# Performance work log

Hardware: AMD Instinct MI355X
Metric: run time of the kernel (lower is better)

Reference implementation:

```python
import jax, jax.numpy as jnp
import numpy as np

B = 256      # batch
D_IN = 784   # input_dims
WIDTH = 256  # block width
DEPTH = 10   # number of fc_relu blocks
NCLS = 10    # num_classes


def setup_inputs() -> dict:
    key = jax.random.key(0)
    ks = jax.random.split(key, 7)
    s1 = 1.0 / np.sqrt(D_IN)
    s2 = 1.0 / np.sqrt(WIDTH)
    x = jax.random.normal(ks[0], (B, D_IN), jnp.float32)
    W1 = jax.random.uniform(ks[1], (WIDTH, D_IN), jnp.float32, -s1, s1)
    b1 = jax.random.uniform(ks[2], (WIDTH,), jnp.float32, -s1, s1)
    Wb = jax.random.uniform(ks[3], (DEPTH, WIDTH, WIDTH), jnp.float32, -s2, s2)
    bb = jax.random.uniform(ks[4], (DEPTH, WIDTH), jnp.float32, -s2, s2)
    Wl = jax.random.uniform(ks[5], (NCLS, WIDTH), jnp.float32, -s2, s2)
    bl = jax.random.uniform(ks[6], (NCLS,), jnp.float32, -s2, s2)
    return dict(x=x, W1=W1, b1=b1, Wb=Wb, bb=bb, Wl=Wl, bl=bl)


def reference(x, W1, b1, Wb, bb, Wl, bl):
    # first_fc + relu
    y = jax.nn.relu(x @ W1.T + b1)                      # [B, WIDTH]
    eye = jnp.eye(WIDTH, dtype=y.dtype)

    def step(y, wb):
        W, b = wb                                       # [WIDTH, WIDTH], [WIDTH]
        # fc_relu.dev(x, skip=True): per-sample Jacobian W @ diag(relu'(x)) + I
        # (W @ diag(d) scales columns of W by d) -- vectorized replacement for
        # the original nested Python-loop diag build.
        mask = (y >= 0).astype(y.dtype)                 # [B, WIDTH]
        J = W[None, :, :] * mask[:, None, :] + eye      # [B, WIDTH, WIDTH]
        sigma = jnp.linalg.svd(J, compute_uv=False)     # [B, WIDTH], descending
        # residual relu block: relu(fc(x)) + x
        y = jax.nn.relu(y @ W.T + b) + y
        return y, sigma

    y, sigmas = jax.lax.scan(step, y, (Wb, bb))         # sigmas: [DEPTH, B, WIDTH]
    # feat_tag='ldi': all_sigma = mean over blocks of sigma_mean
    all_sigma = jnp.mean(sigmas, axis=0)                # [B, WIDTH]
    out = y @ Wl.T + bl                                 # last_fc, [B, NCLS]
    return out, all_sigma
```

## Files before the change

### kernel.cpp

```cpp
#include <hip/hip_runtime.h>
#include <hip/hip_bf16.h>

#define NW 256
#define NDEPTH 10
#define NS 25
#define PAD 12
#define PIV_EPS 1e-6f

__global__ __launch_bounds__(256) void bmat_fwd_kernel(
    const float* __restrict__ Wb, float* __restrict__ Ball, unsigned int* __restrict__ rsmax,
    const float* __restrict__ x, const float* __restrict__ W1, const float* __restrict__ b1,
    const float* __restrict__ bb, const float* __restrict__ Wl, const float* __restrict__ bl,
    float* __restrict__ out) {
  __shared__ __align__(16) float xs[784];
  __shared__ __align__(16) float ybuf[2][NW];
  __shared__ float wsum[4][8];

  if (blockIdx.x < NDEPTH * 32) {
    const int blk = blockIdx.x;
    const int k   = blk >> 5;
    const int r0  = (blk & 31) << 3;
    const int c   = threadIdx.x;
    const float* W = Wb + (size_t)k * NW * NW;
    float acc[8] = {0.f,0.f,0.f,0.f,0.f,0.f,0.f,0.f};
    for (int j = 0; j < NW; ++j) {
      const float wc = W[j * NW + c];
#pragma unroll
      for (int rr = 0; rr < 8; ++rr) acc[rr] += wc * W[j * NW + r0 + rr];
    }
    float a[8];
#pragma unroll
    for (int rr = 0; rr < 8; ++rr) {
      const int r = r0 + rr;
      const float s = acc[rr] + W[c * NW + r] + W[r * NW + c] + ((r == c) ? 1.f : 0.f);
      Ball[(size_t)k * NW * NW + r * NW + c] = s;
      a[rr] = fabsf(s);
    }
#pragma unroll
    for (int off = 32; off; off >>= 1) {
#pragma unroll
      for (int rr = 0; rr < 8; ++rr) a[rr] += __shfl_down(a[rr], off);
    }
    if ((c & 63) == 0) {
#pragma unroll
      for (int rr = 0; rr < 8; ++rr) wsum[c >> 6][rr] = a[rr];
    }
    __syncthreads();
    if (c == 0) {
      float mx = 0.f;
#pragma unroll
      for (int rr = 0; rr < 8; ++rr)
        mx = fmaxf(mx, wsum[0][rr] + wsum[1][rr] + wsum[2][rr] + wsum[3][rr]);
      atomicMax(&rsmax[k], __float_as_uint(mx));
    }
  } else {
    const int b = blockIdx.x - NDEPTH * 32;
    const int o = threadIdx.x;
    for (int k = o; k < 784; k += 256) xs[k] = x[(size_t)b * 784 + k];
    __syncthreads();
    {
      const float* w1r = W1 + (size_t)o * 784;
      float a0 = 0.f, a1 = 0.f, a2 = 0.f, a3 = 0.f;
      for (int k = 0; k < 784; k += 16) {
        const float4 w0 = *(const float4*)(w1r + k);
        const float4 x0 = *(const float4*)(&xs[k]);
        const float4 w1v = *(const float4*)(w1r + k + 4);
        const float4 x1 = *(const float4*)(&xs[k + 4]);
        const float4 w2 = *(const float4*)(w1r + k + 8);
        const float4 x2 = *(const float4*)(&xs[k + 8]);
        const float4 w3 = *(const float4*)(w1r + k + 12);
        const float4 x3 = *(const float4*)(&xs[k + 12]);
        a0 += w0.x*x0.x + w0.y*x0.y + w0.z*x0.z + w0.w*x0.w;
        a1 += w1v.x*x1.x + w1v.y*x1.y + w1v.z*x1.z + w1v.w*x1.w;
        a2 += w2.x*x2.x + w2.y*x2.y + w2.z*x2.z + w2.w*x2.w;
        a3 += w3.x*x3.x + w3.y*x3.y + w3.z*x3.z + w3.w*x3.w;
      }
      ybuf[0][o] = fmaxf(b1[o] + ((a0 + a1) + (a2 + a3)), 0.f);
    }
    __syncthreads();
    int cur = 0;
    for (int d = 0; d < NDEPTH; ++d) {
      const float* wr = Wb + (size_t)d * NW * NW + (size_t)o * NW;
      const float* yc = ybuf[cur];
      float a0 = 0.f, a1 = 0.f, a2 = 0.f, a3 = 0.f;
#pragma unroll 4
      for (int k = 0; k < NW; k += 16) {
        const float4 w0 = *(const float4*)(wr + k);
        const float4 y0 = *(const float4*)(&yc[k]);
        const float4 w1v = *(const float4*)(wr + k + 4);
        const float4 y1 = *(const float4*)(&yc[k + 4]);
        const float4 w2 = *(const float4*)(wr + k + 8);
        const float4 y2 = *(const float4*)(&yc[k + 8]);
        const float4 w3 = *(const float4*)(wr + k + 12);
        const float4 y3 = *(const float4*)(&yc[k + 12]);
        a0 += w0.x*y0.x + w0.y*y0.y + w0.z*y0.z + w0.w*y0.w;
        a1 += w1v.x*y1.x + w1v.y*y1.y + w1v.z*y1.z + w1v.w*y1.w;
        a2 += w2.x*y2.x + w2.y*y2.y + w2.z*y2.z + w2.w*y2.w;
        a3 += w3.x*y3.x + w3.y*y3.y + w3.z*y3.z + w3.w*y3.w;
      }
      const float acc = bb[d * NW + o] + ((a0 + a1) + (a2 + a3));
      const float ynew = fmaxf(acc, 0.f) + yc[o];
      ybuf[cur ^ 1][o] = ynew;
      __syncthreads();
      cur ^= 1;
    }
    if (o < 10) {
      const float* wr = Wl + o * NW;
      const float* yc = ybuf[cur];
      float a0 = 0.f, a1 = 0.f;
      for (int k = 0; k < NW; k += 8) {
        const float4 w0 = *(const float4*)(wr + k);
        const float4 y0 = *(const float4*)(&yc[k]);
        const float4 w1v = *(const float4*)(wr + k + 4);
        const float4 y1 = *(const float4*)(&yc[k + 4]);
        a0 += w0.x*y0.x + w0.y*y0.y + w0.z*y0.z + w0.w*y0.w;
        a1 += w1v.x*y1.x + w1v.y*y1.y + w1v.z*y1.z + w1v.w*y1.w;
      }
      out[b * 10 + o] = bl[o] + a0 + a1;
    }
  }
}

__global__ __launch_bounds__(1024, 4) void ldl_kernel(const float* __restrict__ Ball,
                                                      const unsigned int* __restrict__ rsmax,
                                                      int* __restrict__ counts) {
  const int s   = blockIdx.x;
  const int mat = blockIdx.y;
  const int t = threadIdx.x;
  const int l = t & 63;
  const int w = t >> 6;
  const int rg = l & 31;
  const int ch = 2 * w + (l >> 5);
  const int r0 = rg << 3;

  __shared__ __align__(16) float vrow[2][2][32 * PAD];

  const float h = sqrtf(__uint_as_float(rsmax[mat])) * (1.f / NS);
  const float sg = (s + 1) * h;
  const float mu = sg * sg;

  float Bf[64];
  {
    const float* src = Ball + (size_t)mat * NW * NW + (size_t)r0 * NW + (ch << 3);
#pragma unroll
    for (int i = 0; i < 8; ++i) {
      const float4 a = *(const float4*)(src + i * NW);
      const float4 b = *(const float4*)(src + i * NW + 4);
      Bf[i*8+0] = a.x; Bf[i*8+1] = a.y; Bf[i*8+2] = a.z; Bf[i*8+3] = a.w;
      Bf[i*8+4] = b.x; Bf[i*8+5] = b.y; Bf[i*8+6] = b.z; Bf[i*8+7] = b.w;
    }
  }
  if (rg == ch) {
#pragma unroll
    for (int i = 0; i < 8; ++i) Bf[i*8+i] -= mu;
  }

  if (rg == 0) {
    float* vd0 = &vrow[0][0][ch * PAD];
    float* vd1 = &vrow[0][1][ch * PAD];
    *(float4*)&vd0[0] = make_float4(Bf[0],  Bf[1],  Bf[2],  Bf[3]);
    *(float4*)&vd0[4] = make_float4(Bf[4],  Bf[5],  Bf[6],  Bf[7]);
    *(float4*)&vd1[0] = make_float4(Bf[8],  Bf[9],  Bf[10], Bf[11]);
    *(float4*)&vd1[4] = make_float4(Bf[12], Bf[13], Bf[14], Bf[15]);
  }
  __syncthreads();

  int cnt = 0;
  for (int m = 0; m < NW / 2; ++m) {
    const int k = 2 * m;
    const int par = m & 1;
    const float* v0 = vrow[par][0];
    const float* v1 = vrow[par][1];

    const int kpos = (k >> 3) * PAD + (k & 7);
    const float2 p01 = *(const float2*)&v0[kpos];
    const float d0  = p01.x;
    const float u01 = p01.y;
    const float e1  = v1[kpos + 1];
    const float d0g = (fabsf(d0) < PIV_EPS) ? copysignf(PIV_EPS, d0) : d0;
    const float i0  = __builtin_amdgcn_rcpf(d0g);
    const float l10 = u01 * i0;
    const float d1  = e1 - l10 * u01;
    const float d1g = (fabsf(d1) < PIV_EPS) ? copysignf(PIV_EPS, d1) : d1;
    const float i1  = __builtin_amdgcn_rcpf(d1g);
    cnt += (d0 < 0.f) ? 1 : 0;
    cnt += (d1 < 0.f) ? 1 : 0;

    if (16 * w + 15 > k) {
      const float4 ra0 = *(const float4*)&v0[rg * PAD + 0];
      const float4 ra1 = *(const float4*)&v0[rg * PAD + 4];
      const float4 rb0 = *(const float4*)&v1[rg * PAD + 0];
      const float4 rb1 = *(const float4*)&v1[rg * PAD + 4];
      const float4 ca0 = *(const float4*)&v0[ch * PAD + 0];
      const float4 ca1 = *(const float4*)&v0[ch * PAD + 4];
      const float4 cb0 = *(const float4*)&v1[ch * PAD + 0];
      const float4 cb1 = *(const float4*)&v1[ch * PAD + 4];
      const float rv0[8] = {ra0.x, ra0.y, ra0.z, ra0.w, ra1.x, ra1.y, ra1.z, ra1.w};
      const float rv1[8] = {rb0.x, rb0.y, rb0.z, rb0.w, rb1.x, rb1.y, rb1.z, rb1.w};
      const float cv0[8] = {ca0.x, ca0.y, ca0.z, ca0.w, ca1.x, ca1.y, ca1.z, ca1.w};
      const float cv1[8] = {cb0.x, cb0.y, cb0.z, cb0.w, cb1.x, cb1.y, cb1.z, cb1.w};

      float g0[8], f1[8];
#pragma unroll
      for (int i = 0; i < 8; ++i) {
        const int r = r0 + i;
        const float f0 = (r > k)     ? -rv0[i] * i0 : 0.f;
        const float v1p = rv1[i] - l10 * rv0[i];
        f1[i] = (r > k + 1) ? -v1p * i1 : 0.f;
        g0[i] = f0 - l10 * f1[i];
      }
#pragma unroll
      for (int i = 0; i < 8; ++i) {
#pragma unroll
        for (int j = 0; j < 8; ++j) {
          Bf[i*8+j] = fmaf(g0[i], cv0[j], fmaf(f1[i], cv1[j], Bf[i*8+j]));
        }
      }
      const int nr = k + 2;
      if (nr < NW && rg == (nr >> 3)) {
        float* vd0 = &vrow[par ^ 1][0][ch * PAD];
        float* vd1 = &vrow[par ^ 1][1][ch * PAD];
        switch (nr & 7) {
          case 0:
            *(float4*)&vd0[0] = make_float4(Bf[0],  Bf[1],  Bf[2],  Bf[3]);
            *(float4*)&vd0[4] = make_float4(Bf[4],  Bf[5],  Bf[6],  Bf[7]);
            *(float4*)&vd1[0] = make_float4(Bf[8],  Bf[9],  Bf[10], Bf[11]);
            *(float4*)&vd1[4] = make_float4(Bf[12], Bf[13], Bf[14], Bf[15]);
            break;
          case 2:
            *(float4*)&vd0[0] = make_float4(Bf[16], Bf[17], Bf[18], Bf[19]);
            *(float4*)&vd0[4] = make_float4(Bf[20], Bf[21], Bf[22], Bf[23]);
            *(float4*)&vd1[0] = make_float4(Bf[24], Bf[25], Bf[26], Bf[27]);
            *(float4*)&vd1[4] = make_float4(Bf[28], Bf[29], Bf[30], Bf[31]);
            break;
          case 4:
            *(float4*)&vd0[0] = make_float4(Bf[32], Bf[33], Bf[34], Bf[35]);
            *(float4*)&vd0[4] = make_float4(Bf[36], Bf[37], Bf[38], Bf[39]);
            *(float4*)&vd1[0] = make_float4(Bf[40], Bf[41], Bf[42], Bf[43]);
            *(float4*)&vd1[4] = make_float4(Bf[44], Bf[45], Bf[46], Bf[47]);
            break;
          default:
            *(float4*)&vd0[0] = make_float4(Bf[48], Bf[49], Bf[50], Bf[51]);
            *(float4*)&vd0[4] = make_float4(Bf[52], Bf[53], Bf[54], Bf[55]);
            *(float4*)&vd1[0] = make_float4(Bf[56], Bf[57], Bf[58], Bf[59]);
            *(float4*)&vd1[4] = make_float4(Bf[60], Bf[61], Bf[62], Bf[63]);
            break;
        }
      }
    }
    __syncthreads();
  }

  if (t == 0) counts[mat * NS + s] = cnt;
}

__global__ void gather_out_kernel(const int* __restrict__ counts,
                                  const unsigned int* __restrict__ rsmax,
                                  float* __restrict__ out_all) {
  const int b = blockIdx.x;
  const int j = threadIdx.x;
  float acc = 0.f;
#pragma unroll
  for (int mat = 0; mat < NDEPTH; ++mat) {
    const float h = sqrtf(__uint_as_float(rsmax[mat])) * (1.f / NS);
    int cmax = 0;
    int sstar = NS - 1;
    bool found = false;
    for (int s = 0; s < NS; ++s) {
      cmax = max(cmax, counts[mat * NS + s]);
      if (!found && cmax > (255 - j)) { sstar = s; found = true; }
    }
    acc += (sstar + 0.5f) * h;
  }
  out_all[b * NW + j] = acc * 0.1f;
}

extern "C" void kernel_launch(void* const* d_in, const int* in_sizes, int n_in,
                              void* d_out, int out_size, void* d_ws, size_t ws_size,
                              hipStream_t stream) {
  const float* x  = (const float*)d_in[0];
  const float* W1 = (const float*)d_in[1];
  const float* b1 = (const float*)d_in[2];
  const float* Wb = (const float*)d_in[3];
  const float* bb = (const float*)d_in[4];
  const float* Wl = (const float*)d_in[5];
  const float* bl = (const float*)d_in[6];
  float* out = (float*)d_out;

  float* ws = (float*)d_ws;
  float* Ball   = ws;
  unsigned int* rsmaxW = (unsigned int*)(ws + 655360);
  int*   counts = (int*)(ws + 655376);

  hipMemsetAsync(rsmaxW, 0, NDEPTH * sizeof(unsigned int), stream);
  bmat_fwd_kernel<<<dim3(NDEPTH * 32 + 256), dim3(256), 0, stream>>>(
      Wb, Ball, rsmaxW, x, W1, b1, bb, Wl, bl, out);
  ldl_kernel<<<dim3(NS, NDEPTH), dim3(1024), 0, stream>>>(Ball, rsmaxW, counts);
  gather_out_kernel<<<dim3(256), dim3(256), 0, stream>>>(counts, rsmaxW, out + 2560);
}
```

Measured before the change: 269.4 us.

## Compute next pivot rows early and defer rank-2 update past barrier

In the LDL inertia-count kernel, the thread owning the next pivot rows now updates and publishes only those two rows before the barrier. The full 8x8 rank-2 trailing update is moved after the __syncthreads, so the barrier no longer waits on all threads finishing their FMA block and can overlap with it. The gather kernel also stages the counts table in shared memory instead of reading global memory repeatedly. The cost is extra live registers (g0, f1, cv0, cv1 across the barrier), a duplicated FMA path for the dump rows, and zeroing of coefficients to avoid double-applying the update.

Result: slower. 771.0 us (+186.2%).

```diff
diff --git a/kernel.cpp b/kernel.cpp
--- a/kernel.cpp
+++ b/kernel.cpp
@@ -121,6 +121,19 @@
   }
 }
 
+#define MINI_DUMP(R0) do {                                                          \
+  _Pragma("unroll")                                                                 \
+  for (int j = 0; j < 8; ++j) {                                                     \
+    Bf[(R0)*8+j]   = fmaf(g0[(R0)],   cv0[j], fmaf(f1[(R0)],   cv1[j], Bf[(R0)*8+j]));   \
+    Bf[(R0+1)*8+j] = fmaf(g0[(R0)+1], cv0[j], fmaf(f1[(R0)+1], cv1[j], Bf[(R0+1)*8+j])); \
+  }                                                                                 \
+  *(float4*)&vd0[0] = make_float4(Bf[(R0)*8+0], Bf[(R0)*8+1], Bf[(R0)*8+2], Bf[(R0)*8+3]); \
+  *(float4*)&vd0[4] = make_float4(Bf[(R0)*8+4], Bf[(R0)*8+5], Bf[(R0)*8+6], Bf[(R0)*8+7]); \
+  *(float4*)&vd1[0] = make_float4(Bf[(R0+1)*8+0], Bf[(R0+1)*8+1], Bf[(R0+1)*8+2], Bf[(R0+1)*8+3]); \
+  *(float4*)&vd1[4] = make_float4(Bf[(R0+1)*8+4], Bf[(R0+1)*8+5], Bf[(R0+1)*8+6], Bf[(R0+1)*8+7]); \
+  g0[(R0)] = 0.f; f1[(R0)] = 0.f; g0[(R0)+1] = 0.f; f1[(R0)+1] = 0.f;               \
+} while (0)
+
 __global__ __launch_bounds__(1024, 4) void ldl_kernel(const float* __restrict__ Ball,
                                                       const unsigned int* __restrict__ rsmax,
                                                       int* __restrict__ counts) {
@@ -171,6 +184,7 @@
     const int par = m & 1;
     const float* v0 = vrow[par][0];
     const float* v1 = vrow[par][1];
+    const bool live = (16 * w + 15 > k);
 
     const int kpos = (k >> 3) * PAD + (k & 7);
     const float2 p01 = *(const float2*)&v0[kpos];
@@ -186,7 +200,8 @@
     cnt += (d0 < 0.f) ? 1 : 0;
     cnt += (d1 < 0.f) ? 1 : 0;
 
-    if (16 * w + 15 > k) {
+    float g0[8], f1[8], cv0[8], cv1[8];
+    if (live) {
       const float4 ra0 = *(const float4*)&v0[rg * PAD + 0];
       const float4 ra1 = *(const float4*)&v0[rg * PAD + 4];
       const float4 rb0 = *(const float4*)&v1[rg * PAD + 0];
@@ -197,10 +212,11 @@
       const float4 cb1 = *(const float4*)&v1[ch * PAD + 4];
       const float rv0[8] = {ra0.x, ra0.y, ra0.z, ra0.w, ra1.x, ra1.y, ra1.z, ra1.w};
       const float rv1[8] = {rb0.x, rb0.y, rb0.z, rb0.w, rb1.x, rb1.y, rb1.z, rb1.w};
-      const float cv0[8] = {ca0.x, ca0.y, ca0.z, ca0.w, ca1.x, ca1.y, ca1.z, ca1.w};
-      const float cv1[8] = {cb0.x, cb0.y, cb0.z, cb0.w, cb1.x, cb1.y, cb1.z, cb1.w};
-
-      float g0[8], f1[8];
+      cv0[0]=ca0.x; cv0[1]=ca0.y; cv0[2]=ca0.z; cv0[3]=ca0.w;
+      cv0[4]=ca1.x; cv0[5]=ca1.y; cv0[6]=ca1.z; cv0[7]=ca1.w;
+      cv1[0]=cb0.x; cv1[1]=cb0.y; cv1[2]=cb0.z; cv1[3]=cb0.w;
+      cv1[4]=cb1.x; cv1[5]=cb1.y; cv1[6]=cb1.z; cv1[7]=cb1.w;
+
 #pragma unroll
       for (int i = 0; i < 8; ++i) {
         const int r = r0 + i;
@@ -209,46 +225,30 @@
         f1[i] = (r > k + 1) ? -v1p * i1 : 0.f;
         g0[i] = f0 - l10 * f1[i];
       }
-#pragma unroll
-      for (int i = 0; i < 8; ++i) {
-#pragma unroll
-        for (int j = 0; j < 8; ++j) {
-          Bf[i*8+j] = fmaf(g0[i], cv0[j], fmaf(f1[i], cv1[j], Bf[i*8+j]));
-        }
-      }
+
       const int nr = k + 2;
       if (nr < NW && rg == (nr >> 3)) {
         float* vd0 = &vrow[par ^ 1][0][ch * PAD];
         float* vd1 = &vrow[par ^ 1][1][ch * PAD];
         switch (nr & 7) {
-          case 0:
-            *(float4*)&vd0[0] = make_float4(Bf[0],  Bf[1],  Bf[2],  Bf[3]);
-            *(float4*)&vd0[4] = make_float4(Bf[4],  Bf[5],  Bf[6],  Bf[7]);
-            *(float4*)&vd1[0] = make_float4(Bf[8],  Bf[9],  Bf[10], Bf[11]);
-            *(float4*)&vd1[4] = make_float4(Bf[12], Bf[13], Bf[14], Bf[15]);
-            break;
-          case 2:
-            *(float4*)&vd0[0] = make_float4(Bf[16], Bf[17], Bf[18], Bf[19]);
-            *(float4*)&vd0[4] = make_float4(Bf[20], Bf[21], Bf[22], Bf[23]);
-            *(float4*)&vd1[0] = make_float4(Bf[24], Bf[25], Bf[26], Bf[27]);
-            *(float4*)&vd1[4] = make_float4(Bf[28], Bf[29], Bf[30], Bf[31]);
-            break;
-          case 4:
-            *(float4*)&vd0[0] = make_float4(Bf[32], Bf[33], Bf[34], Bf[35]);
-            *(float4*)&vd0[4] = make_float4(Bf[36], Bf[37], Bf[38], Bf[39]);
-            *(float4*)&vd1[0] = make_float4(Bf[40], Bf[41], Bf[42], Bf[43]);
-            *(float4*)&vd1[4] = make_float4(Bf[44], Bf[45], Bf[46], Bf[47]);
-            break;
-          default:
-            *(float4*)&vd0[0] = make_float4(Bf[48], Bf[49], Bf[50], Bf[51]);
-            *(float4*)&vd0[4] = make_float4(Bf[52], Bf[53], Bf[54], Bf[55]);
-            *(float4*)&vd1[0] = make_float4(Bf[56], Bf[57], Bf[58], Bf[59]);
-            *(float4*)&vd1[4] = make_float4(Bf[60], Bf[61], Bf[62], Bf[63]);
-            break;
+          case 0:  MINI_DUMP(0); break;
+          case 2:  MINI_DUMP(2); break;
+          case 4:  MINI_DUMP(4); break;
+          default: MINI_DUMP(6); break;
         }
       }
     }
     __syncthreads();
+
+    if (live) {
+#pragma unroll
+      for (int i = 0; i < 8; ++i) {
+#pragma unroll
+        for (int j = 0; j < 8; ++j) {
+          Bf[i*8+j] = fmaf(g0[i], cv0[j], fmaf(f1[i], cv1[j], Bf[i*8+j]));
+        }
+      }
+    }
   }
 
   if (t == 0) counts[mat * NS + s] = cnt;
@@ -259,6 +259,9 @@
                                   float* __restrict__ out_all) {
   const int b = blockIdx.x;
   const int j = threadIdx.x;
+  __shared__ int cs[NDEPTH * NS];
+  if (j < NDEPTH * NS) cs[j] = counts[j];
+  __syncthreads();
   float acc = 0.f;
 #pragma unroll
   for (int mat = 0; mat < NDEPTH; ++mat) {
@@ -267,7 +270,7 @@
     int sstar = NS - 1;
     bool found = false;
     for (int s = 0; s < NS; ++s) {
-      cmax = max(cmax, counts[mat * NS + s]);
+      cmax = max(cmax, cs[mat * NS + s]);
       if (!found && cmax > (255 - j)) { sstar = s; found = true; }
     }
     acc += (sstar + 0.5f) * h;
```

## Move forward MLP pass from Gram kernel into LDL kernel's spare blocks

Applied to the files above, without the earlier changes.

The forward residual MLP pass (first FC, ten residual blocks, last FC) moves out of the Gram-matrix kernel and into extra blocks of the LDL inertia-count kernel. Each 1024-thread block now handles four batch rows, giving 64 forward blocks next to the 250 LDL blocks. The goal is to hide the forward work behind the long serial LDL elimination and to shorten the Gram kernel. The gather kernel also stages the counts table in shared memory. In exchange, the LDL kernel now allocates a larger shared buffer sized for the forward path, which may reduce occupancy.

Result: slower. 530.1 us (+96.8%).

```diff
diff --git a/kernel.cpp b/kernel.cpp
--- a/kernel.cpp
+++ b/kernel.cpp
@@ -6,56 +6,194 @@
 #define NS 25
 #define PAD 12
 #define PIV_EPS 1e-6f
-
-__global__ __launch_bounds__(256) void bmat_fwd_kernel(
-    const float* __restrict__ Wb, float* __restrict__ Ball, unsigned int* __restrict__ rsmax,
+#define NLDL (NS * NDEPTH)
+#define NFWD 64
+
+__global__ __launch_bounds__(256) void bmat_kernel(
+    const float* __restrict__ Wb, float* __restrict__ Ball, unsigned int* __restrict__ rsmax) {
+  __shared__ float wsum[4][8];
+  const int blk = blockIdx.x;
+  const int k   = blk >> 5;
+  const int r0  = (blk & 31) << 3;
+  const int c   = threadIdx.x;
+  const float* W = Wb + (size_t)k * NW * NW;
+  float acc[8] = {0.f,0.f,0.f,0.f,0.f,0.f,0.f,0.f};
+  for (int j = 0; j < NW; ++j) {
+    const float wc = W[j * NW + c];
+#pragma unroll
+    for (int rr = 0; rr < 8; ++rr) acc[rr] += wc * W[j * NW + r0 + rr];
+  }
+  float a[8];
+#pragma unroll
+  for (int rr = 0; rr < 8; ++rr) {
+    const int r = r0 + rr;
+    const float s = acc[rr] + W[c * NW + r] + W[r * NW + c] + ((r == c) ? 1.f : 0.f);
+    Ball[(size_t)k * NW * NW + r * NW + c] = s;
+    a[rr] = fabsf(s);
+  }
+#pragma unroll
+  for (int off = 32; off; off >>= 1) {
+#pragma unroll
+    for (int rr = 0; rr < 8; ++rr) a[rr] += __shfl_down(a[rr], off);
+  }
+  if ((c & 63) == 0) {
+#pragma unroll
+    for (int rr = 0; rr < 8; ++rr) wsum[c >> 6][rr] = a[rr];
+  }
+  __syncthreads();
+  if (c == 0) {
+    float mx = 0.f;
+#pragma unroll
+    for (int rr = 0; rr < 8; ++rr)
+      mx = fmaxf(mx, wsum[0][rr] + wsum[1][rr] + wsum[2][rr] + wsum[3][rr]);
+    atomicMax(&rsmax[k], __float_as_uint(mx));
+  }
+}
+
+__global__ __launch_bounds__(1024, 4) void ldl_fwd_kernel(
+    const float* __restrict__ Ball, const unsigned int* __restrict__ rsmax,
+    int* __restrict__ counts,
     const float* __restrict__ x, const float* __restrict__ W1, const float* __restrict__ b1,
-    const float* __restrict__ bb, const float* __restrict__ Wl, const float* __restrict__ bl,
+    const float* __restrict__ Wb, const float* __restrict__ bb,
+    const float* __restrict__ Wl, const float* __restrict__ bl,
     float* __restrict__ out) {
-  __shared__ __align__(16) float xs[784];
-  __shared__ __align__(16) float ybuf[2][NW];
-  __shared__ float wsum[4][8];
-
-  if (blockIdx.x < NDEPTH * 32) {
-    const int blk = blockIdx.x;
-    const int k   = blk >> 5;
-    const int r0  = (blk & 31) << 3;
-    const int c   = threadIdx.x;
-    const float* W = Wb + (size_t)k * NW * NW;
-    float acc[8] = {0.f,0.f,0.f,0.f,0.f,0.f,0.f,0.f};
-    for (int j = 0; j < NW; ++j) {
-      const float wc = W[j * NW + c];
-#pragma unroll
-      for (int rr = 0; rr < 8; ++rr) acc[rr] += wc * W[j * NW + r0 + rr];
-    }
-    float a[8];
-#pragma unroll
-    for (int rr = 0; rr < 8; ++rr) {
-      const int r = r0 + rr;
-      const float s = acc[rr] + W[c * NW + r] + W[r * NW + c] + ((r == c) ? 1.f : 0.f);
-      Ball[(size_t)k * NW * NW + r * NW + c] = s;
-      a[rr] = fabsf(s);
-    }
-#pragma unroll
-    for (int off = 32; off; off >>= 1) {
-#pragma unroll
-      for (int rr = 0; rr < 8; ++rr) a[rr] += __shfl_down(a[rr], off);
-    }
-    if ((c & 63) == 0) {
-#pragma unroll
-      for (int rr = 0; rr < 8; ++rr) wsum[c >> 6][rr] = a[rr];
+  __shared__ __align__(16) float smem[4 * 784 + 4 * 2 * NW];
+  const int t = threadIdx.x;
+
+  if (blockIdx.x < NLDL) {
+    const int s   = blockIdx.x % NS;
+    const int mat = blockIdx.x / NS;
+    const int l = t & 63;
+    const int w = t >> 6;
+    const int rg = l & 31;
+    const int ch = 2 * w + (l >> 5);
+    const int r0 = rg << 3;
+    float* vrow = smem;
+
+    const float h = sqrtf(__uint_as_float(rsmax[mat])) * (1.f / NS);
+    const float sg = (s + 1) * h;
+    const float mu = sg * sg;
+
+    float Bf[64];
+    {
+      const float* src = Ball + (size_t)mat * NW * NW + (size_t)r0 * NW + (ch << 3);
+#pragma unroll
+      for (int i = 0; i < 8; ++i) {
+        const float4 a = *(const float4*)(src + i * NW);
+        const float4 b = *(const float4*)(src + i * NW + 4);
+        Bf[i*8+0] = a.x; Bf[i*8+1] = a.y; Bf[i*8+2] = a.z; Bf[i*8+3] = a.w;
+        Bf[i*8+4] = b.x; Bf[i*8+5] = b.y; Bf[i*8+6] = b.z; Bf[i*8+7] = b.w;
+      }
+    }
+    if (rg == ch) {
+#pragma unroll
+      for (int i = 0; i < 8; ++i) Bf[i*8+i] -= mu;
+    }
+
+    if (rg == 0) {
+      float* vd0 = &vrow[0 * 384 + ch * PAD];
+      float* vd1 = &vrow[1 * 384 + ch * PAD];
+      *(float4*)&vd0[0] = make_float4(Bf[0],  Bf[1],  Bf[2],  Bf[3]);
+      *(float4*)&vd0[4] = make_float4(Bf[4],  Bf[5],  Bf[6],  Bf[7]);
+      *(float4*)&vd1[0] = make_float4(Bf[8],  Bf[9],  Bf[10], Bf[11]);
+      *(float4*)&vd1[4] = make_float4(Bf[12], Bf[13], Bf[14], Bf[15]);
     }
     __syncthreads();
-    if (c == 0) {
-      float mx = 0.f;
-#pragma unroll
-      for (int rr = 0; rr < 8; ++rr)
-        mx = fmaxf(mx, wsum[0][rr] + wsum[1][rr] + wsum[2][rr] + wsum[3][rr]);
-      atomicMax(&rsmax[k], __float_as_uint(mx));
-    }
+
+    int cnt = 0;
+    for (int m = 0; m < NW / 2; ++m) {
+      const int k = 2 * m;
+      const int par = m & 1;
+      const float* v0 = &vrow[(par * 2 + 0) * 384];
+      const float* v1 = &vrow[(par * 2 + 1) * 384];
+
+      const int kpos = (k >> 3) * PAD + (k & 7);
+      const float2 p01 = *(const float2*)&v0[kpos];
+      const float d0  = p01.x;
+      const float u01 = p01.y;
+      const float e1  = v1[kpos + 1];
+      const float d0g = (fabsf(d0) < PIV_EPS) ? copysignf(PIV_EPS, d0) : d0;
+      const float i0  = __builtin_amdgcn_rcpf(d0g);
+      const float l10 = u01 * i0;
+      const float d1  = e1 - l10 * u01;
+      const float d1g = (fabsf(d1) < PIV_EPS) ? copysignf(PIV_EPS, d1) : d1;
+      const float i1  = __builtin_amdgcn_rcpf(d1g);
+      cnt += (d0 < 0.f) ? 1 : 0;
+      cnt += (d1 < 0.f) ? 1 : 0;
+
+      if (16 * w + 15 > k) {
+        const float4 ra0 = *(const float4*)&v0[rg * PAD + 0];
+        const float4 ra1 = *(const float4*)&v0[rg * PAD + 4];
+        const float4 rb0 = *(const float4*)&v1[rg * PAD + 0];
+        const float4 rb1 = *(const float4*)&v1[rg * PAD + 4];
+        const float4 ca0 = *(const float4*)&v0[ch * PAD + 0];
+        const float4 ca1 = *(const float4*)&v0[ch * PAD + 4];
+        const float4 cb0 = *(const float4*)&v1[ch * PAD + 0];
+        const float4 cb1 = *(const float4*)&v1[ch * PAD + 4];
+        const float rv0[8] = {ra0.x, ra0.y, ra0.z, ra0.w, ra1.x, ra1.y, ra1.z, ra1.w};
+        const float rv1[8] = {rb0.x, rb0.y, rb0.z, rb0.w, rb1.x, rb1.y, rb1.z, rb1.w};
+        const float cv0[8] = {ca0.x, ca0.y, ca0.z, ca0.w, ca1.x, ca1.y, ca1.z, ca1.w};
+        const float cv1[8] = {cb0.x, cb0.y, cb0.z, cb0.w, cb1.x, cb1.y, cb1.z, cb1.w};
+
+        float g0[8], f1[8];
+#pragma unroll
+        for (int i = 0; i < 8; ++i) {
+          const int r = r0 + i;
+          const float f0 = (r > k)     ? -rv0[i] * i0 : 0.f;
+          const float v1p = rv1[i] - l10 * rv0[i];
+          f1[i] = (r > k + 1) ? -v1p * i1 : 0.f;
+          g0[i] = f0 - l10 * f1[i];
+        }
+#pragma unroll
+        for (int i = 0; i < 8; ++i) {
+#pragma unroll
+          for (int j = 0; j < 8; ++j) {
+            Bf[i*8+j] = fmaf(g0[i], cv0[j], fmaf(f1[i], cv1[j], Bf[i*8+j]));
+          }
+        }
+        const int nr = k + 2;
+        if (nr < NW && rg == (nr >> 3)) {
+          float* vd0 = &vrow[((par ^ 1) * 2 + 0) * 384 + ch * PAD];
+          float* vd1 = &vrow[((par ^ 1) * 2 + 1) * 384 + ch * PAD];
+          switch (nr & 7) {
+            case 0:
+              *(float4*)&vd0[0] = make_float4(Bf[0],  Bf[1],  Bf[2],  Bf[3]);
+              *(float4*)&vd0[4] = make_float4(Bf[4],  Bf[5],  Bf[6],  Bf[7]);
+              *(float4*)&vd1[0] = make_float4(Bf[8],  Bf[9],  Bf[10], Bf[11]);
+              *(float4*)&vd1[4] = make_float4(Bf[12], Bf[13], Bf[14], Bf[15]);
+              break;
+            case 2:
+              *(float4*)&vd0[0] = make_float4(Bf[16], Bf[17], Bf[18], Bf[19]);
+              *(float4*)&vd0[4] = make_float4(Bf[20], Bf[21], Bf[22], Bf[23]);
+              *(float4*)&vd1[0] = make_float4(Bf[24], Bf[25], Bf[26], Bf[27]);
+              *(float4*)&vd1[4] = make_float4(Bf[28], Bf[29], Bf[30], Bf[31]);
+              break;
+            case 4:
+              *(float4*)&vd0[0] = make_float4(Bf[32], Bf[33], Bf[34], Bf[35]);
+              *(float4*)&vd0[4] = make_float4(Bf[36], Bf[37], Bf[38], Bf[39]);
+              *(float4*)&vd1[0] = make_float4(Bf[40], Bf[41], Bf[42], Bf[43]);
+              *(float4*)&vd1[4] = make_float4(Bf[44], Bf[45], Bf[46], Bf[47]);
+              break;
+            default:
+              *(float4*)&vd0[0] = make_float4(Bf[48], Bf[49], Bf[50], Bf[51]);
+              *(float4*)&vd0[4] = make_float4(Bf[52], Bf[53], Bf[54], Bf[55]);
+              *(float4*)&vd1[0] = make_float4(Bf[56], Bf[57], Bf[58], Bf[59]);
+              *(float4*)&vd1[4] = make_float4(Bf[60], Bf[61], Bf[62], Bf[63]);
+              break;
+          }
+        }
+      }
+      __syncthreads();
+    }
+
+    if (t == 0) counts[mat * NS + s] = cnt;
   } else {
-    const int b = blockIdx.x - NDEPTH * 32;
-    const int o = threadIdx.x;
+    const int grp = t >> 8;
+    const int o = t & 255;
+    const int b = 4 * (blockIdx.x - NLDL) + grp;
+    float* xs = &smem[grp * 784];
+    float* yb = &smem[4 * 784 + grp * 2 * NW];
+
     for (int k = o; k < 784; k += 256) xs[k] = x[(size_t)b * 784 + k];
     __syncthreads();
     {
@@ -75,13 +213,13 @@
         a2 += w2.x*x2.x + w2.y*x2.y + w2.z*x2.z + w2.w*x2.w;
         a3 += w3.x*x3.x + w3.y*x3.y + w3.z*x3.z + w3.w*x3.w;
       }
-      ybuf[0][o] = fmaxf(b1[o] + ((a0 + a1) + (a2 + a3)), 0.f);
+      yb[o] = fmaxf(b1[o] + ((a0 + a1) + (a2 + a3)), 0.f);
     }
     __syncthreads();
     int cur = 0;
     for (int d = 0; d < NDEPTH; ++d) {
       const float* wr = Wb + (size_t)d * NW * NW + (size_t)o * NW;
-      const float* yc = ybuf[cur];
+      const float* yc = &yb[cur * NW];
       float a0 = 0.f, a1 = 0.f, a2 = 0.f, a3 = 0.f;
 #pragma unroll 4
       for (int k = 0; k < NW; k += 16) {
@@ -100,13 +238,13 @@
       }
       const float acc = bb[d * NW + o] + ((a0 + a1) + (a2 + a3));
       const float ynew = fmaxf(acc, 0.f) + yc[o];
-      ybuf[cur ^ 1][o] = ynew;
+      yb[(cur ^ 1) * NW + o] = ynew;
       __syncthreads();
       cur ^= 1;
     }
     if (o < 10) {
       const float* wr = Wl + o * NW;
-      const float* yc = ybuf[cur];
+      const float* yc = &yb[cur * NW];
       float a0 = 0.f, a1 = 0.f;
       for (int k = 0; k < NW; k += 8) {
         const float4 w0 = *(const float4*)(wr + k);
@@ -121,144 +259,14 @@
   }
 }
 
-__global__ __launch_bounds__(1024, 4) void ldl_kernel(const float* __restrict__ Ball,
-                                                      const unsigned int* __restrict__ rsmax,
-                                                      int* __restrict__ counts) {
-  const int s   = blockIdx.x;
-  const int mat = blockIdx.y;
-  const int t = threadIdx.x;
-  const int l = t & 63;
-  const int w = t >> 6;
-  const int rg = l & 31;
-  const int ch = 2 * w + (l >> 5);
-  const int r0 = rg << 3;
-
-  __shared__ __align__(16) float vrow[2][2][32 * PAD];
-
-  const float h = sqrtf(__uint_as_float(rsmax[mat])) * (1.f / NS);
-  const float sg = (s + 1) * h;
-  const float mu = sg * sg;
-
-  float Bf[64];
-  {
-    const float* src = Ball + (size_t)mat * NW * NW + (size_t)r0 * NW + (ch << 3);
-#pragma unroll
-    for (int i = 0; i < 8; ++i) {
-      const float4 a = *(const float4*)(src + i * NW);
-      const float4 b = *(const float4*)(src + i * NW + 4);
-      Bf[i*8+0] = a.x; Bf[i*8+1] = a.y; Bf[i*8+2] = a.z; Bf[i*8+3] = a.w;
-      Bf[i*8+4] = b.x; Bf[i*8+5] = b.y; Bf[i*8+6] = b.z; Bf[i*8+7] = b.w;
-    }
-  }
-  if (rg == ch) {
-#pragma unroll
-    for (int i = 0; i < 8; ++i) Bf[i*8+i] -= mu;
-  }
-
-  if (rg == 0) {
-    float* vd0 = &vrow[0][0][ch * PAD];
-    float* vd1 = &vrow[0][1][ch * PAD];
-    *(float4*)&vd0[0] = make_float4(Bf[0],  Bf[1],  Bf[2],  Bf[3]);
-    *(float4*)&vd0[4] = make_float4(Bf[4],  Bf[5],  Bf[6],  Bf[7]);
-    *(float4*)&vd1[0] = make_float4(Bf[8],  Bf[9],  Bf[10], Bf[11]);
-    *(float4*)&vd1[4] = make_float4(Bf[12], Bf[13], Bf[14], Bf[15]);
-  }
-  __syncthreads();
-
-  int cnt = 0;
-  for (int m = 0; m < NW / 2; ++m) {
-    const int k = 2 * m;
-    const int par = m & 1;
-    const float* v0 = vrow[par][0];
-    const float* v1 = vrow[par][1];
-
-    const int kpos = (k >> 3) * PAD + (k & 7);
-    const float2 p01 = *(const float2*)&v0[kpos];
-    const float d0  = p01.x;
-    const float u01 = p01.y;
-    const float e1  = v1[kpos + 1];
-    const float d0g = (fabsf(d0) < PIV_EPS) ? copysignf(PIV_EPS, d0) : d0;
-    const float i0  = __builtin_amdgcn_rcpf(d0g);
-    const float l10 = u01 * i0;
-    const float d1  = e1 - l10 * u01;
-    const float d1g = (fabsf(d1) < PIV_EPS) ? copysignf(PIV_EPS, d1) : d1;
-    const float i1  = __builtin_amdgcn_rcpf(d1g);
-    cnt += (d0 < 0.f) ? 1 : 0;
-    cnt += (d1 < 0.f) ? 1 : 0;
-
-    if (16 * w + 15 > k) {
-      const float4 ra0 = *(const float4*)&v0[rg * PAD + 0];
-      const float4 ra1 = *(const float4*)&v0[rg * PAD + 4];
-      const float4 rb0 = *(const float4*)&v1[rg * PAD + 0];
-      const float4 rb1 = *(const float4*)&v1[rg * PAD + 4];
-      const float4 ca0 = *(const float4*)&v0[ch * PAD + 0];
-      const float4 ca1 = *(const float4*)&v0[ch * PAD + 4];
-      const float4 cb0 = *(const float4*)&v1[ch * PAD + 0];
-      const float4 cb1 = *(const float4*)&v1[ch * PAD + 4];
-      const float rv0[8] = {ra0.x, ra0.y, ra0.z, ra0.w, ra1.x, ra1.y, ra1.z, ra1.w};
-      const float rv1[8] = {rb0.x, rb0.y, rb0.z, rb0.w, rb1.x, rb1.y, rb1.z, rb1.w};
-      const float cv0[8] = {ca0.x, ca0.y, ca0.z, ca0.w, ca1.x, ca1.y, ca1.z, ca1.w};
-      const float cv1[8] = {cb0.x, cb0.y, cb0.z, cb0.w, cb1.x, cb1.y, cb1.z, cb1.w};
-
-      float g0[8], f1[8];
-#pragma unroll
-      for (int i = 0; i < 8; ++i) {
-        const int r = r0 + i;
-        const float f0 = (r > k)     ? -rv0[i] * i0 : 0.f;
-        const float v1p = rv1[i] - l10 * rv0[i];
-        f1[i] = (r > k + 1) ? -v1p * i1 : 0.f;
-        g0[i] = f0 - l10 * f1[i];
-      }
-#pragma unroll
-      for (int i = 0; i < 8; ++i) {
-#pragma unroll
-        for (int j = 0; j < 8; ++j) {
-          Bf[i*8+j] = fmaf(g0[i], cv0[j], fmaf(f1[i], cv1[j], Bf[i*8+j]));
-        }
-      }
-      const int nr = k + 2;
-      if (nr < NW && rg == (nr >> 3)) {
-        float* vd0 = &vrow[par ^ 1][0][ch * PAD];
-        float* vd1 = &vrow[par ^ 1][1][ch * PAD];
-        switch (nr & 7) {
-          case 0:
-            *(float4*)&vd0[0] = make_float4(Bf[0],  Bf[1],  Bf[2],  Bf[3]);
-            *(float4*)&vd0[4] = make_float4(Bf[4],  Bf[5],  Bf[6],  Bf[7]);
-            *(float4*)&vd1[0] = make_float4(Bf[8],  Bf[9],  Bf[10], Bf[11]);
-            *(float4*)&vd1[4] = make_float4(Bf[12], Bf[13], Bf[14], Bf[15]);
-            break;
-          case 2:
-            *(float4*)&vd0[0] = make_float4(Bf[16], Bf[17], Bf[18], Bf[19]);
-            *(float4*)&vd0[4] = make_float4(Bf[20], Bf[21], Bf[22], Bf[23]);
-            *(float4*)&vd1[0] = make_float4(Bf[24], Bf[25], Bf[26], Bf[27]);
-            *(float4*)&vd1[4] = make_float4(Bf[28], Bf[29], Bf[30], Bf[31]);
-            break;
-          case 4:
-            *(float4*)&vd0[0] = make_float4(Bf[32], Bf[33], Bf[34], Bf[35]);
-            *(float4*)&vd0[4] = make_float4(Bf[36], Bf[37], Bf[38], Bf[39]);
-            *(float4*)&vd1[0] = make_float4(Bf[40], Bf[41], Bf[42], Bf[43]);
-            *(float4*)&vd1[4] = make_float4(Bf[44], Bf[45], Bf[46], Bf[47]);
-            break;
-          default:
-            *(float4*)&vd0[0] = make_float4(Bf[48], Bf[49], Bf[50], Bf[51]);
-            *(float4*)&vd0[4] = make_float4(Bf[52], Bf[53], Bf[54], Bf[55]);
-            *(float4*)&vd1[0] = make_float4(Bf[56], Bf[57], Bf[58], Bf[59]);
-            *(float4*)&vd1[4] = make_float4(Bf[60], Bf[61], Bf[62], Bf[63]);
-            break;
-        }
-      }
-    }
-    __syncthreads();
-  }
-
-  if (t == 0) counts[mat * NS + s] = cnt;
-}
-
 __global__ void gather_out_kernel(const int* __restrict__ counts,
                                   const unsigned int* __restrict__ rsmax,
                                   float* __restrict__ out_all) {
   const int b = blockIdx.x;
   const int j = threadIdx.x;
+  __shared__ int cs[NDEPTH * NS];
+  if (j < NDEPTH * NS) cs[j] = counts[j];
+  __syncthreads();
   float acc = 0.f;
 #pragma unroll
   for (int mat = 0; mat < NDEPTH; ++mat) {
@@ -267,7 +275,7 @@
     int sstar = NS - 1;
     bool found = false;
     for (int s = 0; s < NS; ++s) {
-      cmax = max(cmax, counts[mat * NS + s]);
+      cmax = max(cmax, cs[mat * NS + s]);
       if (!found && cmax > (255 - j)) { sstar = s; found = true; }
     }
     acc += (sstar + 0.5f) * h;
@@ -293,8 +301,8 @@
   int*   counts = (int*)(ws + 655376);
 
   hipMemsetAsync(rsmaxW, 0, NDEPTH * sizeof(unsigned int), stream);
-  bmat_fwd_kernel<<<dim3(NDEPTH * 32 + 256), dim3(256), 0, stream>>>(
-      Wb, Ball, rsmaxW, x, W1, b1, bb, Wl, bl, out);
-  ldl_kernel<<<dim3(NS, NDEPTH), dim3(1024), 0, stream>>>(Ball, rsmaxW, counts);
+  bmat_kernel<<<dim3(NDEPTH * 32), dim3(256), 0, stream>>>(Wb, Ball, rsmaxW);
+  ldl_fwd_kernel<<<dim3(NLDL + NFWD), dim3(1024), 0, stream>>>(
+      Ball, rsmaxW, counts, x, W1, b1, Wb, bb, Wl, bl, out);
   gather_out_kernel<<<dim3(256), dim3(256), 0, stream>>>(counts, rsmaxW, out + 2560);
 }
```
